# Kernel tuning notes

Hardware: AMD Instinct MI355X
Metric: run time of the kernel (lower is better)

Reference implementation:

```python
import jax, jax.numpy as jnp
import numpy as np

C = 256

def setup_inputs() -> dict:
    key = jax.random.key(0)
    ks = jax.random.split(key, 8)
    B, H, W = 4, 64, 64
    x = jax.random.normal(ks[0], (B, C, H, W), dtype=jnp.float32)
    # 1x1 conv weights ~ kaiming uniform; bias zero
    bound = np.sqrt(6.0 / C)
    Wq = jax.random.uniform(ks[1], (C, C), minval=-bound, maxval=bound, dtype=jnp.float32)
    Wk = jax.random.uniform(ks[2], (C, C), minval=-bound, maxval=bound, dtype=jnp.float32)
    Wv = jax.random.uniform(ks[3], (C, C), minval=-bound, maxval=bound, dtype=jnp.float32)
    bq = jnp.zeros((C,), jnp.float32)
    bk = jnp.zeros((C,), jnp.float32)
    bv = jnp.zeros((C,), jnp.float32)
    # gamma initialized to zero in torch; use small nonzero so output depends on attn path
    gamma = jnp.array([0.1], dtype=jnp.float32)
    return {"x": x, "Wq": Wq, "bq": bq, "Wk": Wk, "bk": bk, "Wv": Wv, "bv": bv, "gamma": gamma}


def reference(x, Wq, bq, Wk, bk, Wv, bv, gamma):
    B, Cc, H, W = x.shape
    N = H * W
    xf = x.reshape(B, Cc, N)  # [B,C,N]
    # 1x1 conv == per-pixel linear over channels: out[b,o,n] = sum_c W[o,c]*x[b,c,n] + b[o]
    q = jnp.einsum('oc,bcn->bon', Wq, xf) + bq[None, :, None]  # [B,C,N]
    k = jnp.einsum('oc,bcn->bon', Wk, xf) + bk[None, :, None]
    v = jnp.einsum('oc,bcn->bon', Wv, xf) + bv[None, :, None]
    # energy[b,i,j] = q[b,:,i] . k[b,:,j]  (no scaling, as in source)
    energy = jnp.einsum('bci,bcj->bij', q, k)  # [B,N,N]
    attention = jax.nn.softmax(energy, axis=-1)
    # out[b,c,i] = sum_j v[b,c,j] * attention[b,i,j]  (bmm(value, attn^T))
    out = jnp.einsum('bcj,bij->bci', v, attention)
    out = out.reshape(B, Cc, H, W)
    return gamma * out + x
```

## Files before the change

### kernel.cpp

```cpp
#include <hip/hip_runtime.h>
#include <hip/hip_bf16.h>
#include <cstdint>


#define C_DIM 256
#define N_DIM 4096
#define B_DIM 4

typedef _Float16 f16;
typedef f16 f16x8 __attribute__((ext_vector_type(8)));
typedef f16 f16x4 __attribute__((ext_vector_type(4)));
typedef float f32x4 __attribute__((ext_vector_type(4)));

__device__ __forceinline__ void dma16(const f16* g, f16* l) {
  __builtin_amdgcn_global_load_lds(
      (const __attribute__((address_space(1))) unsigned int*)g,
      (__attribute__((address_space(3))) unsigned int*)l, 16, 0, 0);
}

__global__ __launch_bounds__(256) void k_prep_xs(const float* __restrict__ x,
                                                 f16* __restrict__ xs) {
  __shared__ float tile[64][65];
  const int b = blockIdx.z, nb = blockIdx.x * 64, cb = blockIdx.y * 64;
  const float* xb = x + (size_t)b * C_DIM * N_DIM;
  for (int i = threadIdx.x; i < 64 * 64; i += 256) {
    int c = i >> 6, n = i & 63;
    tile[c][n] = xb[(size_t)(cb + c) * N_DIM + nb + n];
  }
  __syncthreads();
  f16* xsb = xs + (size_t)b * N_DIM * C_DIM;
  for (int i = threadIdx.x; i < 64 * 64; i += 256) {
    int n = i >> 6, c = i & 63;
    xsb[(size_t)(nb + n) * C_DIM + cb + c] = (f16)tile[c][n];
  }
}

__global__ __launch_bounds__(256) void k_cast_w(const float* __restrict__ Wq,
                                                const float* __restrict__ Wk,
                                                const float* __restrict__ Wv,
                                                f16* __restrict__ Wh) {
  int i = blockIdx.x * 256 + threadIdx.x;
  int sel = i >> 16, j = i & 65535;
  const float* s = (sel == 0) ? Wq : (sel == 1) ? Wk : Wv;
  Wh[i] = (f16)s[j];
}

__global__ __launch_bounds__(256) void k_proj(const f16* __restrict__ xs,
                                              const f16* __restrict__ Wh,
                                              const float* __restrict__ bq,
                                              const float* __restrict__ bk,
                                              const float* __restrict__ bv,
                                              f16* __restrict__ Qh,
                                              f16* __restrict__ Kh,
                                              f16* __restrict__ Vh) {
  const int z = blockIdx.y;
  const int w = threadIdx.x >> 6, lane = threadIdx.x & 63;
  const int quad = lane >> 4, li = lane & 15;
  const f16* W = Wh + (size_t)z * 65536;
  const float* bias = (z == 0) ? bq : (z == 1) ? bk : bv;

  if (z < 2) {
    f16* out = (z == 0) ? Qh : Kh;
    const int g0 = (blockIdx.x * 4 + w) * 16;
    f16x8 a[8];
    const f16* arow = xs + (size_t)(g0 + li) * C_DIM + quad * 8;
#pragma unroll
    for (int kf = 0; kf < 8; kf++) a[kf] = *(const f16x8*)(arow + kf * 32);
    for (int ot = 0; ot < 16; ot++) {
      f32x4 acc = {0.f, 0.f, 0.f, 0.f};
      const f16* brow = W + (size_t)(ot * 16 + li) * C_DIM + quad * 8;
#pragma unroll
      for (int kf = 0; kf < 8; kf++) {
        f16x8 bf = *(const f16x8*)(brow + kf * 32);
        acc = __builtin_amdgcn_mfma_f32_16x16x32_f16(a[kf], bf, acc, 0, 0, 0);
      }
      float bb = bias[ot * 16 + li];
      f16* orow = out + (size_t)g0 * C_DIM + ot * 16 + li;
#pragma unroll
      for (int r = 0; r < 4; r++)
        orow[(size_t)(quad * 4 + r) * C_DIM] = (f16)(acc[r] + bb);
    }
  } else {
    const int t = blockIdx.x * 4 + w;
    const int b = t >> 8, j0 = (t & 255) * 16;
    f16x8 bfr[8];
    const f16* brow = xs + (size_t)(b * N_DIM + j0 + li) * C_DIM + quad * 8;
#pragma unroll
    for (int kf = 0; kf < 8; kf++) bfr[kf] = *(const f16x8*)(brow + kf * 32);
    for (int ot = 0; ot < 16; ot++) {
      f32x4 acc = {0.f, 0.f, 0.f, 0.f};
      const f16* arow = W + (size_t)(ot * 16 + li) * C_DIM + quad * 8;
#pragma unroll
      for (int kf = 0; kf < 8; kf++) {
        f16x8 af = *(const f16x8*)(arow + kf * 32);
        acc = __builtin_amdgcn_mfma_f32_16x16x32_f16(af, bfr[kf], acc, 0, 0, 0);
      }
      f16* obase = Vh + ((size_t)(b * C_DIM + ot * 16 + quad * 4)) * N_DIM + j0 + li;
#pragma unroll
      for (int r = 0; r < 4; r++) {
        float bb = bias[ot * 16 + quad * 4 + r];
        obase[(size_t)r * N_DIM] = (f16)(acc[r] + bb);
      }
    }
  }
}

#define JT 64
#define NT (N_DIM / JT)
#define KBUF 16896
#define VBUF 16896
#define K0_OFF 0
#define K1_OFF 16896
#define V0_OFF 33792
#define V1_OFF 50688
#define P_OFF  67584
#define PSTR 80
#define SMEM_F16 72704

__global__ __launch_bounds__(256, 1) void k_attn(const f16* __restrict__ Qh,
                                                 const f16* __restrict__ Kh,
                                                 const f16* __restrict__ Vh,
                                                 const float* __restrict__ x,
                                                 const float* __restrict__ gamma_p,
                                                 float* __restrict__ out) {
  __shared__ __align__(16) f16 smem[SMEM_F16];
  const int b = blockIdx.y;
  const int tid = threadIdx.x;
  const int w = tid >> 6, lane = tid & 63;
  const int quad = lane >> 4, li = lane & 15;
  const int ibase = blockIdx.x * 64 + w * 16;

  f16x8 qf[8];
  {
    const f16* qrow = Qh + (size_t)(b * N_DIM + ibase + li) * C_DIM + quad * 8;
#pragma unroll
    for (int kf = 0; kf < 8; kf++) qf[kf] = *(const f16x8*)(qrow + kf * 32);
  }
  const f16* Kb = Kh + (size_t)b * N_DIM * C_DIM;
  const f16* Vb = Vh + (size_t)b * C_DIM * N_DIM;
  f16* Pw = smem + P_OFF + w * 16 * PSTR;

  const float LOG2E = 1.4426950408889634f;
  float m = -3.0e38f, l = 0.0f;
  f32x4 acc[16];
#pragma unroll
  for (int ct = 0; ct < 16; ct++) acc[ct] = (f32x4){0.f, 0.f, 0.f, 0.f};

  {
    const f16* kg = Kb;
    const f16* vg = Vb;
#pragma unroll
    for (int it = 0; it < 8; it++) {
      int p = w * 8 + it;
      dma16(kg + (size_t)(2 * p + (lane >> 5)) * C_DIM + (lane & 31) * 8,
            smem + K0_OFF + p * 528);
      dma16(vg + (size_t)(p * 8 + (lane >> 3)) * N_DIM + (lane & 7) * 8,
            smem + V0_OFF + p * 528);
    }
  }
  __syncthreads();

  for (int t = 0; t < NT; t++) {
    const f16* Kc = smem + ((t & 1) ? K1_OFF : K0_OFF);
    const f16* Vc = smem + ((t & 1) ? V1_OFF : V0_OFF);

    if (t + 1 < NT) {
      f16* Kn = smem + ((t & 1) ? K0_OFF : K1_OFF);
      f16* Vn = smem + ((t & 1) ? V0_OFF : V1_OFF);
      const int jt = (t + 1) * JT;
      const f16* kg = Kb + (size_t)jt * C_DIM;
      const f16* vg = Vb + jt;
#pragma unroll
      for (int it = 0; it < 8; it++) {
        int p = w * 8 + it;
        dma16(kg + (size_t)(2 * p + (lane >> 5)) * C_DIM + (lane & 31) * 8,
              Kn + p * 528);
        dma16(vg + (size_t)(p * 8 + (lane >> 3)) * N_DIM + (lane & 7) * 8,
              Vn + p * 528);
      }
    }

    f32x4 s[4];
#pragma unroll
    for (int sub = 0; sub < 4; sub++) {
      f32x4 ss = {0.f, 0.f, 0.f, 0.f};
      const int r = sub * 16 + li;
      const f16* krow = Kc + (r >> 1) * 528 + (r & 1) * 256 + quad * 8;
#pragma unroll
      for (int kf = 0; kf < 8; kf++) {
        f16x8 kfr = *(const f16x8*)(krow + kf * 32);
        ss = __builtin_amdgcn_mfma_f32_16x16x32_f16(kfr, qf[kf], ss, 0, 0, 0);
      }
      s[sub] = ss;
    }

    float tm = -3.0e38f;
#pragma unroll
    for (int sub = 0; sub < 4; sub++)
      tm = fmaxf(tm, fmaxf(fmaxf(s[sub][0], s[sub][1]), fmaxf(s[sub][2], s[sub][3])));
    tm = fmaxf(tm, __shfl_xor(tm, 16));
    tm = fmaxf(tm, __shfl_xor(tm, 32));
    float nm = fmaxf(m, tm);
    float alpha = exp2f((m - nm) * LOG2E);
    m = nm;
    if (__any(alpha < 1.0f)) {
      l *= alpha;
#pragma unroll
      for (int ct = 0; ct < 16; ct++) {
        acc[ct][0] *= alpha; acc[ct][1] *= alpha;
        acc[ct][2] *= alpha; acc[ct][3] *= alpha;
      }
    }
#pragma unroll
    for (int sub = 0; sub < 4; sub++) {
      float p0 = exp2f((s[sub][0] - m) * LOG2E);
      float p1 = exp2f((s[sub][1] - m) * LOG2E);
      float p2 = exp2f((s[sub][2] - m) * LOG2E);
      float p3 = exp2f((s[sub][3] - m) * LOG2E);
      l += (p0 + p1) + (p2 + p3);
      *(f16x4*)(Pw + li * PSTR + sub * 16 + quad * 4) =
          (f16x4){(f16)p0, (f16)p1, (f16)p2, (f16)p3};
    }

    f16x8 pf0 = *(const f16x8*)(Pw + li * PSTR + quad * 8);
    f16x8 pf1 = *(const f16x8*)(Pw + li * PSTR + 32 + quad * 8);
#pragma unroll
    for (int ct = 0; ct < 16; ct++) {
      const f16* vrow = Vc + (ct * 2 + (li >> 3)) * 528 + (li & 7) * 64 + quad * 8;
      f16x8 v0 = *(const f16x8*)(vrow);
      f16x8 v1 = *(const f16x8*)(vrow + 32);
      acc[ct] = __builtin_amdgcn_mfma_f32_16x16x32_f16(v0, pf0, acc[ct], 0, 0, 0);
      acc[ct] = __builtin_amdgcn_mfma_f32_16x16x32_f16(v1, pf1, acc[ct], 0, 0, 0);
    }

    __syncthreads();
  }

  l += __shfl_xor(l, 16);
  l += __shfl_xor(l, 32);
  const float scale = gamma_p[0] / l;

  const float* xb = x + (size_t)b * C_DIM * N_DIM;
  float* ob = out + (size_t)b * C_DIM * N_DIM;
  const int icol = ibase + li;
#pragma unroll
  for (int ct = 0; ct < 16; ct++) {
#pragma unroll
    for (int r = 0; r < 4; r++) {
      size_t off = (size_t)(ct * 16 + quad * 4 + r) * N_DIM + icol;
      ob[off] = acc[ct][r] * scale + xb[off];
    }
  }
}

extern "C" void kernel_launch(void* const* d_in, const int* in_sizes, int n_in,
                              void* d_out, int out_size, void* d_ws, size_t ws_size,
                              hipStream_t stream) {
  const float* x     = (const float*)d_in[0];
  const float* Wq    = (const float*)d_in[1];
  const float* bq    = (const float*)d_in[2];
  const float* Wk    = (const float*)d_in[3];
  const float* bk    = (const float*)d_in[4];
  const float* Wv    = (const float*)d_in[5];
  const float* bv    = (const float*)d_in[6];
  const float* gamma = (const float*)d_in[7];
  float* out = (float*)d_out;

  char* ws = (char*)d_ws;
  f16* xs = (f16*)(ws);
  f16* Qh = (f16*)(ws + (size_t)8  * 1024 * 1024);
  f16* Kh = (f16*)(ws + (size_t)16 * 1024 * 1024);
  f16* Vh = (f16*)(ws + (size_t)24 * 1024 * 1024);
  f16* Wh = (f16*)(ws + (size_t)32 * 1024 * 1024);

  k_prep_xs<<<dim3(64, 4, 4), 256, 0, stream>>>(x, xs);
  k_cast_w<<<dim3(768), 256, 0, stream>>>(Wq, Wk, Wv, Wh);
  k_proj<<<dim3(256, 3), 256, 0, stream>>>(xs, Wh, bq, bk, bv, Qh, Kh, Vh);
  k_attn<<<dim3(64, 4), 256, 0, stream>>>(Qh, Kh, Vh, x, gamma, out);
}
```

Measured before the change: 299.5 us.

## Split attention keys across waves with direct global loads and cross-wave merge

The attention kernel now gives each block only 16 query rows. Its four waves each process a quarter of the keys (split-K style), and the partial softmax states and accumulators are merged through LDS at the end. The LDS double-buffered DMA staging of K/V is removed: waves read K and V fragments straight from global memory, which relies on L2/MALL reuse. Grid size rises fourfold and launch_bounds allows 3 blocks per SM. The projection kernel also splits output tiles across wave pairs to double its grid. The trade is more K/V traffic per query and a reduction epilogue, in exchange for more parallelism and occupancy.

```diff
diff --git a/kernel.cpp b/kernel.cpp
--- a/kernel.cpp
+++ b/kernel.cpp
@@ -11,12 +11,6 @@
 typedef f16 f16x8 __attribute__((ext_vector_type(8)));
 typedef f16 f16x4 __attribute__((ext_vector_type(4)));
 typedef float f32x4 __attribute__((ext_vector_type(4)));
-
-__device__ __forceinline__ void dma16(const f16* g, f16* l) {
-  __builtin_amdgcn_global_load_lds(
-      (const __attribute__((address_space(1))) unsigned int*)g,
-      (__attribute__((address_space(3))) unsigned int*)l, 16, 0, 0);
-}
 
 __global__ __launch_bounds__(256) void k_prep_xs(const float* __restrict__ x,
                                                  f16* __restrict__ xs) {
@@ -56,17 +50,18 @@
   const int z = blockIdx.y;
   const int w = threadIdx.x >> 6, lane = threadIdx.x & 63;
   const int quad = lane >> 4, li = lane & 15;
+  const int oh = w & 1;
   const f16* W = Wh + (size_t)z * 65536;
   const float* bias = (z == 0) ? bq : (z == 1) ? bk : bv;
 
   if (z < 2) {
     f16* out = (z == 0) ? Qh : Kh;
-    const int g0 = (blockIdx.x * 4 + w) * 16;
+    const int g0 = blockIdx.x * 32 + (w >> 1) * 16;
     f16x8 a[8];
     const f16* arow = xs + (size_t)(g0 + li) * C_DIM + quad * 8;
 #pragma unroll
     for (int kf = 0; kf < 8; kf++) a[kf] = *(const f16x8*)(arow + kf * 32);
-    for (int ot = 0; ot < 16; ot++) {
+    for (int ot = oh * 8; ot < oh * 8 + 8; ot++) {
       f32x4 acc = {0.f, 0.f, 0.f, 0.f};
       const f16* brow = W + (size_t)(ot * 16 + li) * C_DIM + quad * 8;
 #pragma unroll
@@ -81,13 +76,13 @@
         orow[(size_t)(quad * 4 + r) * C_DIM] = (f16)(acc[r] + bb);
     }
   } else {
-    const int t = blockIdx.x * 4 + w;
+    const int t = blockIdx.x * 2 + (w >> 1);
     const int b = t >> 8, j0 = (t & 255) * 16;
     f16x8 bfr[8];
     const f16* brow = xs + (size_t)(b * N_DIM + j0 + li) * C_DIM + quad * 8;
 #pragma unroll
     for (int kf = 0; kf < 8; kf++) bfr[kf] = *(const f16x8*)(brow + kf * 32);
-    for (int ot = 0; ot < 16; ot++) {
+    for (int ot = oh * 8; ot < oh * 8 + 8; ot++) {
       f32x4 acc = {0.f, 0.f, 0.f, 0.f};
       const f16* arow = W + (size_t)(ot * 16 + li) * C_DIM + quad * 8;
 #pragma unroll
@@ -105,19 +100,13 @@
   }
 }
 
-#define JT 64
-#define NT (N_DIM / JT)
-#define KBUF 16896
-#define VBUF 16896
-#define K0_OFF 0
-#define K1_OFF 16896
-#define V0_OFF 33792
-#define V1_OFF 50688
-#define P_OFF  67584
-#define PSTR 80
-#define SMEM_F16 72704
-
-__global__ __launch_bounds__(256, 1) void k_attn(const f16* __restrict__ Qh,
+#define PSTR 40
+#define P_LDS_F16 (4 * 16 * PSTR)
+#define MX_OFF P_LDS_F16
+#define BUF_OFF (P_LDS_F16 + 256)
+#define SMEM_F16 (P_LDS_F16 + 256 + 8192)
+
+__global__ __launch_bounds__(256, 3) void k_attn(const f16* __restrict__ Qh,
                                                  const f16* __restrict__ Kh,
                                                  const f16* __restrict__ Vh,
                                                  const float* __restrict__ x,
@@ -128,127 +117,124 @@
   const int tid = threadIdx.x;
   const int w = tid >> 6, lane = tid & 63;
   const int quad = lane >> 4, li = lane & 15;
-  const int ibase = blockIdx.x * 64 + w * 16;
+  const int q0 = blockIdx.x * 16;
+
+  const f16* Kb = Kh + (size_t)b * N_DIM * C_DIM;
+  const f16* Vb = Vh + (size_t)b * C_DIM * N_DIM;
+  f16* Pw = smem + w * 16 * PSTR;
+  float* mx = (float*)(smem + MX_OFF);
+  float* buf = (float*)(smem + BUF_OFF);
 
   f16x8 qf[8];
   {
-    const f16* qrow = Qh + (size_t)(b * N_DIM + ibase + li) * C_DIM + quad * 8;
+    const f16* qrow = Qh + (size_t)(b * N_DIM + q0 + li) * C_DIM + quad * 8;
 #pragma unroll
     for (int kf = 0; kf < 8; kf++) qf[kf] = *(const f16x8*)(qrow + kf * 32);
   }
-  const f16* Kb = Kh + (size_t)b * N_DIM * C_DIM;
-  const f16* Vb = Vh + (size_t)b * C_DIM * N_DIM;
-  f16* Pw = smem + P_OFF + w * 16 * PSTR;
-
-  const float LOG2E = 1.4426950408889634f;
+
   float m = -3.0e38f, l = 0.0f;
   f32x4 acc[16];
 #pragma unroll
   for (int ct = 0; ct < 16; ct++) acc[ct] = (f32x4){0.f, 0.f, 0.f, 0.f};
 
-  {
-    const f16* kg = Kb;
-    const f16* vg = Vb;
-#pragma unroll
-    for (int it = 0; it < 8; it++) {
-      int p = w * 8 + it;
-      dma16(kg + (size_t)(2 * p + (lane >> 5)) * C_DIM + (lane & 31) * 8,
-            smem + K0_OFF + p * 528);
-      dma16(vg + (size_t)(p * 8 + (lane >> 3)) * N_DIM + (lane & 7) * 8,
-            smem + V0_OFF + p * 528);
-    }
-  }
-  __syncthreads();
-
-  for (int t = 0; t < NT; t++) {
-    const f16* Kc = smem + ((t & 1) ? K1_OFF : K0_OFF);
-    const f16* Vc = smem + ((t & 1) ? V1_OFF : V0_OFF);
-
-    if (t + 1 < NT) {
-      f16* Kn = smem + ((t & 1) ? K0_OFF : K1_OFF);
-      f16* Vn = smem + ((t & 1) ? V0_OFF : V1_OFF);
-      const int jt = (t + 1) * JT;
-      const f16* kg = Kb + (size_t)jt * C_DIM;
-      const f16* vg = Vb + jt;
-#pragma unroll
-      for (int it = 0; it < 8; it++) {
-        int p = w * 8 + it;
-        dma16(kg + (size_t)(2 * p + (lane >> 5)) * C_DIM + (lane & 31) * 8,
-              Kn + p * 528);
-        dma16(vg + (size_t)(p * 8 + (lane >> 3)) * N_DIM + (lane & 7) * 8,
-              Vn + p * 528);
-      }
-    }
-
-    f32x4 s[4];
-#pragma unroll
-    for (int sub = 0; sub < 4; sub++) {
+  const int kt0 = w * 1024;
+  for (int t = 0; t < 32; t++) {
+    const int keybase = kt0 + t * 32;
+
+    f32x4 s[2];
+#pragma unroll
+    for (int sub = 0; sub < 2; sub++) {
+      const f16* ka = Kb + (size_t)(keybase + sub * 16 + li) * C_DIM + quad * 8;
       f32x4 ss = {0.f, 0.f, 0.f, 0.f};
-      const int r = sub * 16 + li;
-      const f16* krow = Kc + (r >> 1) * 528 + (r & 1) * 256 + quad * 8;
 #pragma unroll
       for (int kf = 0; kf < 8; kf++) {
-        f16x8 kfr = *(const f16x8*)(krow + kf * 32);
+        f16x8 kfr = *(const f16x8*)(ka + kf * 32);
         ss = __builtin_amdgcn_mfma_f32_16x16x32_f16(kfr, qf[kf], ss, 0, 0, 0);
       }
       s[sub] = ss;
     }
 
-    float tm = -3.0e38f;
-#pragma unroll
-    for (int sub = 0; sub < 4; sub++)
-      tm = fmaxf(tm, fmaxf(fmaxf(s[sub][0], s[sub][1]), fmaxf(s[sub][2], s[sub][3])));
+    float tm = fmaxf(fmaxf(fmaxf(s[0][0], s[0][1]), fmaxf(s[0][2], s[0][3])),
+                     fmaxf(fmaxf(s[1][0], s[1][1]), fmaxf(s[1][2], s[1][3])));
     tm = fmaxf(tm, __shfl_xor(tm, 16));
     tm = fmaxf(tm, __shfl_xor(tm, 32));
     float nm = fmaxf(m, tm);
-    float alpha = exp2f((m - nm) * LOG2E);
+    float al = __expf(m - nm);
+    bool upd = nm > m;
     m = nm;
-    if (__any(alpha < 1.0f)) {
-      l *= alpha;
-#pragma unroll
-      for (int ct = 0; ct < 16; ct++) {
-        acc[ct][0] *= alpha; acc[ct][1] *= alpha;
-        acc[ct][2] *= alpha; acc[ct][3] *= alpha;
-      }
-    }
-#pragma unroll
-    for (int sub = 0; sub < 4; sub++) {
-      float p0 = exp2f((s[sub][0] - m) * LOG2E);
-      float p1 = exp2f((s[sub][1] - m) * LOG2E);
-      float p2 = exp2f((s[sub][2] - m) * LOG2E);
-      float p3 = exp2f((s[sub][3] - m) * LOG2E);
+    if (__any(upd)) {
+      l *= al;
+#pragma unroll
+      for (int ct = 0; ct < 16; ct++) acc[ct] *= al;
+    }
+#pragma unroll
+    for (int sub = 0; sub < 2; sub++) {
+      float p0 = __expf(s[sub][0] - m);
+      float p1 = __expf(s[sub][1] - m);
+      float p2 = __expf(s[sub][2] - m);
+      float p3 = __expf(s[sub][3] - m);
       l += (p0 + p1) + (p2 + p3);
       *(f16x4*)(Pw + li * PSTR + sub * 16 + quad * 4) =
           (f16x4){(f16)p0, (f16)p1, (f16)p2, (f16)p3};
     }
 
-    f16x8 pf0 = *(const f16x8*)(Pw + li * PSTR + quad * 8);
-    f16x8 pf1 = *(const f16x8*)(Pw + li * PSTR + 32 + quad * 8);
+    f16x8 pf = *(const f16x8*)(Pw + li * PSTR + quad * 8);
 #pragma unroll
     for (int ct = 0; ct < 16; ct++) {
-      const f16* vrow = Vc + (ct * 2 + (li >> 3)) * 528 + (li & 7) * 64 + quad * 8;
-      f16x8 v0 = *(const f16x8*)(vrow);
-      f16x8 v1 = *(const f16x8*)(vrow + 32);
-      acc[ct] = __builtin_amdgcn_mfma_f32_16x16x32_f16(v0, pf0, acc[ct], 0, 0, 0);
-      acc[ct] = __builtin_amdgcn_mfma_f32_16x16x32_f16(v1, pf1, acc[ct], 0, 0, 0);
-    }
-
-    __syncthreads();
+      const f16* va = Vb + (size_t)(ct * 16 + li) * N_DIM + keybase + quad * 8;
+      f16x8 vf = *(const f16x8*)(va);
+      acc[ct] = __builtin_amdgcn_mfma_f32_16x16x32_f16(vf, pf, acc[ct], 0, 0, 0);
+    }
   }
 
   l += __shfl_xor(l, 16);
   l += __shfl_xor(l, 32);
-  const float scale = gamma_p[0] / l;
-
+  if (lane < 16) {
+    mx[w * 16 + lane] = m;
+    mx[64 + w * 16 + lane] = l;
+  }
+  __syncthreads();
+  float mg = fmaxf(fmaxf(mx[0 + li], mx[16 + li]), fmaxf(mx[32 + li], mx[48 + li]));
+  float lg = __expf(mx[0 + li] - mg) * mx[64 + li] +
+             __expf(mx[16 + li] - mg) * mx[80 + li] +
+             __expf(mx[32 + li] - mg) * mx[96 + li] +
+             __expf(mx[48 + li] - mg) * mx[112 + li];
+  float aw = __expf(m - mg);
+#pragma unroll
+  for (int ct = 0; ct < 16; ct++) acc[ct] *= aw;
+
+#pragma unroll
+  for (int r = 1; r < 4; r++) {
+    const int dest = (w + r) & 3;
+    __syncthreads();
+#pragma unroll
+    for (int cl = 0; cl < 4; cl++) {
+      int ct = dest * 4 + cl;
+#pragma unroll
+      for (int rr = 0; rr < 4; rr++)
+        buf[dest * 1024 + (cl * 16 + quad * 4 + rr) * 16 + li] = acc[ct][rr];
+    }
+    __syncthreads();
+#pragma unroll
+    for (int cl = 0; cl < 4; cl++) {
+      int ct = w * 4 + cl;
+#pragma unroll
+      for (int rr = 0; rr < 4; rr++)
+        acc[ct][rr] += buf[w * 1024 + (cl * 16 + quad * 4 + rr) * 16 + li];
+    }
+  }
+
+  const float scale = gamma_p[0] / lg;
   const float* xb = x + (size_t)b * C_DIM * N_DIM;
   float* ob = out + (size_t)b * C_DIM * N_DIM;
-  const int icol = ibase + li;
-#pragma unroll
-  for (int ct = 0; ct < 16; ct++) {
-#pragma unroll
-    for (int r = 0; r < 4; r++) {
-      size_t off = (size_t)(ct * 16 + quad * 4 + r) * N_DIM + icol;
-      ob[off] = acc[ct][r] * scale + xb[off];
+#pragma unroll
+  for (int cl = 0; cl < 4; cl++) {
+    int ct = w * 4 + cl;
+#pragma unroll
+    for (int rr = 0; rr < 4; rr++) {
+      int ch = ct * 16 + quad * 4 + rr;
+      size_t off = (size_t)ch * N_DIM + q0 + li;
+      ob[off] = acc[ct][rr] * scale + xb[off];
     }
   }
 }
@@ -275,6 +261,6 @@
 
   k_prep_xs<<<dim3(64, 4, 4), 256, 0, stream>>>(x, xs);
   k_cast_w<<<dim3(768), 256, 0, stream>>>(Wq, Wk, Wv, Wh);
-  k_proj<<<dim3(256, 3), 256, 0, stream>>>(xs, Wh, bq, bk, bv, Qh, Kh, Vh);
-  k_attn<<<dim3(64, 4), 256, 0, stream>>>(Qh, Kh, Vh, x, gamma, out);
-}
+  k_proj<<<dim3(512, 3), 256, 0, stream>>>(xs, Wh, bq, bk, bv, Qh, Kh, Vh);
+  k_attn<<<dim3(256, 4), 256, 0, stream>>>(Qh, Kh, Vh, x, gamma, out);
+}
```

Result: slower. 674.2 us (+125.1%).
